# Kernel optimization log

Hardware: AMD Instinct MI355X
Metric: run time of the kernel (lower is better)

The kernel has to match this reference:

```python
import jax, jax.numpy as jnp
import numpy as np

DIM = 768
NUM_HEADS = 12
HEAD_DIM = DIM // NUM_HEADS
SCALE = HEAD_DIM ** -0.5
B, N = 8, 1024


def setup_inputs() -> dict:
    key = jax.random.key(0)
    k1, k2, k3, k4, k5 = jax.random.split(key, 5)
    x = jax.random.normal(k1, (B, N, DIM), dtype=jnp.float32)
    # qkv: Linear(dim, 3*dim, bias=False); proj: Linear(dim, dim) with bias
    w_qkv = jax.random.normal(k2, (3 * DIM, DIM), dtype=jnp.float32) * (DIM ** -0.5)
    w_proj = jax.random.normal(k3, (DIM, DIM), dtype=jnp.float32) * (DIM ** -0.5)
    b_proj = jnp.zeros((DIM,), dtype=jnp.float32)
    # learned attention mask parameter, shape (H, L, L) with L >= N
    att_mask = jax.random.normal(k4, (NUM_HEADS, N, N), dtype=jnp.float32)
    return {"x": x, "w_qkv": w_qkv, "w_proj": w_proj, "b_proj": b_proj, "att_mask": att_mask}


def reference(x, w_qkv, w_proj, b_proj, att_mask):
    Bx, Nx, C = x.shape
    # qkv projection -> (3, B, H, N, head_dim)
    qkv = (x @ w_qkv.T).reshape(Bx, Nx, 3, NUM_HEADS, C // NUM_HEADS)
    qkv = jnp.transpose(qkv, (2, 0, 3, 1, 4))
    q, k, v = qkv[0], qkv[1], qkv[2]  # gpd_ratio==active_ratio==1 -> scaling factor 1
    # scores [B, H, N, N]
    attn = jnp.einsum('bhnd,bhmd->bhnm', q, k) * SCALE
    # custom sigmoid mask gating before softmax (broadcast over batch)
    attn = attn * jax.nn.sigmoid(att_mask[:, :Nx, :Nx])[None, :, :, :]
    attn = jax.nn.softmax(attn, axis=-1)
    out = jnp.einsum('bhnm,bhmd->bhnd', attn, v)
    out = jnp.transpose(out, (0, 2, 1, 3)).reshape(Bx, Nx, C)
    return out @ w_proj.T + b_proj
```

## Files before the change

### kernel.cpp

```cpp
#include <hip/hip_runtime.h>
#include <math.h>
#include <stdint.h>

typedef unsigned short u16;
typedef __attribute__((ext_vector_type(8))) short short8;
typedef __attribute__((ext_vector_type(4))) float f32x4;

#define GATE_SCALE 0.18033688011112042f

#if __has_builtin(__builtin_amdgcn_exp2f)
#define FEXP2(x) __builtin_amdgcn_exp2f(x)
#else
#define FEXP2(x) exp2f(x)
#endif

__device__ __forceinline__ u16 f2b(float f) {
    union { float f; unsigned u; } v; v.f = f;
    unsigned r = v.u + 0x7fffu + ((v.u >> 16) & 1u);
    return (u16)(r >> 16);
}
__device__ __forceinline__ u16 f2b_hu(float f) {
    union { float f; unsigned u; } v; v.f = f;
    return (u16)((v.u + 0x8000u) >> 16);
}
__device__ __forceinline__ float b2f(u16 u) {
    union { float f; unsigned u; } v; v.u = ((unsigned)u) << 16; return v.f;
}

#define GLL16(gsrc, ldsbase) __builtin_amdgcn_global_load_lds(                    \
    (__attribute__((address_space(1))) void*)(uintptr_t)(gsrc),                   \
    (__attribute__((address_space(3))) void*)(uint32_t)(uintptr_t)(ldsbase),      \
    16, 0, 0)

#define NX4  1572864
#define NW14 442368
#define NW24 147456
#define NXW4 (NX4 + NW14 + NW24)

__global__ __launch_bounds__(256) void prep_all(
    const float4* __restrict__ x, const float4* __restrict__ wq,
    const float4* __restrict__ wp,
    ushort4* __restrict__ xb, ushort4* __restrict__ wqb,
    ushort4* __restrict__ wpb,
    const float4* __restrict__ mask4, u16* __restrict__ gp)
{
    __shared__ u16 L[64][72];
    const int bx = blockIdx.x;
    const int t = threadIdx.x;

    if (bx >= 3072) {
        size_t i = (size_t)(bx - 3072) * 256 + t;
        float4 v; ushort4* dst; size_t j;
        if (i < NX4)            { j = i;               v = x[j];  dst = xb;  }
        else if (i < NX4 + NW14){ j = i - NX4;         v = wq[j]; dst = wqb; }
        else                    { j = i - (NX4 + NW14);v = wp[j]; dst = wpb; }
        ushort4 o; o.x = f2b(v.x); o.y = f2b(v.y); o.z = f2b(v.z); o.w = f2b(v.w);
        dst[j] = o;
        return;
    }

    const int bid = bx;
    const int kt = bid & 15, qt = (bid >> 4) & 15, h = bid >> 8;

    #pragma unroll
    for (int s = 0; s < 4; ++s) {
        const int idx = t + s * 256;
        const int row = idx >> 4, c4 = idx & 15;
        float4 v = mask4[(size_t)(h * 1024 + qt * 64 + row) * 256 + kt * 16 + c4];
        L[row][c4 * 4 + 0] = f2b(GATE_SCALE / (1.f + __expf(-v.x)));
        L[row][c4 * 4 + 1] = f2b(GATE_SCALE / (1.f + __expf(-v.y)));
        L[row][c4 * 4 + 2] = f2b(GATE_SCALE / (1.f + __expf(-v.z)));
        L[row][c4 * 4 + 3] = f2b(GATE_SCALE / (1.f + __expf(-v.w)));
    }
    __syncthreads();

    const int w = t >> 6, l = t & 63;
    const int fq = l >> 4, fr = l & 15;
    union { u16 u[16]; float4 f[2]; } vals;
    #pragma unroll
    for (int i = 0; i < 4; ++i)
        #pragma unroll
        for (int nt = 0; nt < 4; ++nt)
            vals.u[i * 4 + nt] = L[16 * w + 4 * fq + i][nt * 16 + fr];
    float4* dst = (float4*)(gp + (size_t)bid * 4096 + (size_t)t * 16);
    dst[0] = vals.f[0];
    dst[1] = vals.f[1];
}

__global__ __launch_bounds__(256) void qkv_gemm(
    const u16* __restrict__ xb, const u16* __restrict__ wb,
    u16* __restrict__ qb, u16* __restrict__ kb, u16* __restrict__ vb)
{
    __shared__ u16 As[2][4096];
    __shared__ u16 Bs[2][4096];
    const int t = threadIdx.x, l = t & 63, w = t >> 6;
    const int wm = (w & 1) * 64, wn = (w >> 1) * 64;

    const int orig = blockIdx.x + 18 * blockIdx.y;
    const int nid = (orig & 7) * 144 + (orig >> 3);
    const int m0 = (nid / 18) * 128, c0 = (nid % 18) * 128;

    f32x4 acc[4][4];
    #pragma unroll
    for (int i = 0; i < 4; ++i)
        #pragma unroll
        for (int j = 0; j < 4; ++j) { f32x4 z = {0.f,0.f,0.f,0.f}; acc[i][j] = z; }

    const int srow = l >> 2, sseg = l & 3;
    const int gcol = ((sseg ^ ((srow >> 1) & 3)) << 3);
    const u16* a0 = xb + (size_t)(m0 + w * 16 + srow) * 768 + gcol;
    const u16* a1 = a0 + (size_t)64 * 768;
    const u16* b0p = wb + (size_t)(c0 + w * 16 + srow) * 768 + gcol;
    const u16* b1p = b0p + (size_t)64 * 768;
    const int wofs = w * 512;

    const int fr = l & 15, fq = l >> 4;
    const int fseg = (fq ^ ((fr >> 1) & 3)) << 3;

    auto stage = [&](int bi, int koff) {
        GLL16(a0 + koff, &As[bi][wofs]);
        GLL16(a1 + koff, &As[bi][2048 + wofs]);
        GLL16(b0p + koff, &Bs[bi][wofs]);
        GLL16(b1p + koff, &Bs[bi][2048 + wofs]);
    };

    stage(0, 0);

    for (int kt = 0; kt < 24; ++kt) {
        asm volatile("s_waitcnt vmcnt(0)" ::: "memory");
        __builtin_amdgcn_s_barrier();
        if (kt < 23) stage((kt + 1) & 1, (kt + 1) * 32);
        const u16* A = As[kt & 1];
        const u16* B = Bs[kt & 1];
        short8 af[4], bf[4];
        #pragma unroll
        for (int mt = 0; mt < 4; ++mt)
            af[mt] = *(const short8*)&A[(wm + mt * 16 + fr) * 32 + fseg];
        #pragma unroll
        for (int nt = 0; nt < 4; ++nt)
            bf[nt] = *(const short8*)&B[(wn + nt * 16 + fr) * 32 + fseg];
        #pragma unroll
        for (int mt = 0; mt < 4; ++mt)
            #pragma unroll
            for (int nt = 0; nt < 4; ++nt)
                acc[mt][nt] = __builtin_amdgcn_mfma_f32_16x16x32_bf16(
                    af[mt], bf[nt], acc[mt][nt], 0, 0, 0);
    }

    const int b = m0 >> 10;
    const int n0 = m0 & 1023;
    #pragma unroll
    for (int nt = 0; nt < 4; ++nt) {
        const int c = c0 + wn + nt * 16 + fr;
        const int which = c / 768;
        const int rem = c - which * 768;
        const int h = rem >> 6, d = rem & 63;
        if (which < 2) {
            u16* dst = ((which == 0) ? qb : kb)
                       + ((size_t)(b * 12 + h) * 1024) * 64 + d;
            #pragma unroll
            for (int mt = 0; mt < 4; ++mt)
                #pragma unroll
                for (int r = 0; r < 4; ++r) {
                    const int n = n0 + wm + mt * 16 + fq * 4 + r;
                    dst[(size_t)n * 64] = f2b(acc[mt][nt][r]);
                }
        } else {
            u16* dst = vb + ((size_t)(b * 12 + h) * 64 + d) * 1024
                          + n0 + wm + fq * 4;
            #pragma unroll
            for (int mt = 0; mt < 4; ++mt) {
                ushort4 pk;
                pk.x = f2b(acc[mt][nt][0]); pk.y = f2b(acc[mt][nt][1]);
                pk.z = f2b(acc[mt][nt][2]); pk.w = f2b(acc[mt][nt][3]);
                *(ushort4*)(dst + mt * 16) = pk;
            }
        }
    }
}

__global__ __launch_bounds__(256, 3) void flash_attn(
    const u16* __restrict__ qb, const u16* __restrict__ kb,
    const u16* __restrict__ vt, const u16* __restrict__ gperm,
    u16* __restrict__ aob)
{
    __shared__ u16 Ks[2][4096], Vts[2][4096], Ps[4096];
    const int t = threadIdx.x, l = t & 63, w = t >> 6;
    const int bid = blockIdx.x;
    const int xcd = bid & 7, jj = bid >> 3;
    const int bh = (jj % 12) * 8 + xcd;
    const int qtb = jj / 12;
    const int h = bh % 12, b = bh / 12;
    const int q0 = qtb * 128;

    const u16* hq = qb + (size_t)bh * 65536;
    const u16* hk = kb + (size_t)bh * 65536;
    const u16* hv = vt + (size_t)bh * 65536;
    const u16* hgb = gperm + ((size_t)h * 256 + qtb * 32) * 4096 + (w * 64 + l) * 16;

    const int sr = l >> 3, ss = l & 7;
    const int sg = ((ss ^ (sr & 7)) << 3);
    const int j0 = w * 2, j1 = j0 + 1;

    const int fq = l >> 4, fr = l & 15;
    const int sega = ((fq ^ (fr & 7)) << 3);
    const int segb = (((4 + fq) ^ (fr & 7)) << 3);

    short8 aq[2][2];
    #pragma unroll
    for (int qh = 0; qh < 2; ++qh) {
        const u16* qrow = hq + (size_t)(q0 + qh * 64 + 16 * w + fr) * 64;
        aq[qh][0] = *(const short8*)(qrow + fq * 8);
        aq[qh][1] = *(const short8*)(qrow + 32 + fq * 8);
    }

    GLL16(hk + (size_t)(j0 * 8 + sr) * 64 + sg, &Ks[0][j0 * 512]);
    GLL16(hk + (size_t)(j1 * 8 + sr) * 64 + sg, &Ks[0][j1 * 512]);
    GLL16(hv + (size_t)(j0 * 8 + sr) * 1024 + sg, &Vts[0][j0 * 512]);
    GLL16(hv + (size_t)(j1 * 8 + sr) * 1024 + sg, &Vts[0][j1 * 512]);
    __builtin_amdgcn_sched_barrier(0);

    short8 gn[4];
    gn[0] = *(const short8*)(hgb);
    gn[1] = *(const short8*)(hgb + 8);
    gn[2] = *(const short8*)(hgb + 65536);
    gn[3] = *(const short8*)(hgb + 65536 + 8);

    float l_part[2][4] = {{0.f,0.f,0.f,0.f},{0.f,0.f,0.f,0.f}};
    f32x4 o[2][4];
    #pragma unroll
    for (int qh = 0; qh < 2; ++qh)
        #pragma unroll
        for (int nt = 0; nt < 4; ++nt) { f32x4 z = {0.f,0.f,0.f,0.f}; o[qh][nt] = z; }

    for (int kt = 0; kt < 16; ++kt) {
        asm volatile("s_waitcnt vmcnt(4)" ::: "memory");
        __builtin_amdgcn_s_barrier();

        if (kt < 15) {
            const size_t ko = (size_t)(kt + 1) * 64;
            u16* kd = &Ks[(kt + 1) & 1][0];
            u16* vd = &Vts[(kt + 1) & 1][0];
            GLL16(hk + (ko + j0 * 8 + sr) * 64 + sg, kd + j0 * 512);
            GLL16(hk + (ko + j1 * 8 + sr) * 64 + sg, kd + j1 * 512);
            GLL16(hv + (size_t)(j0 * 8 + sr) * 1024 + ko + sg, vd + j0 * 512);
            GLL16(hv + (size_t)(j1 * 8 + sr) * 1024 + ko + sg, vd + j1 * 512);
            __builtin_amdgcn_sched_barrier(0);
        }

        short8 g[4];
        #pragma unroll
        for (int s = 0; s < 4; ++s) g[s] = gn[s];
        if (kt < 15) {
            const size_t go = (size_t)(kt + 1) * 4096;
            gn[0] = *(const short8*)(hgb + go);
            gn[1] = *(const short8*)(hgb + go + 8);
            gn[2] = *(const short8*)(hgb + 65536 + go);
            gn[3] = *(const short8*)(hgb + 65536 + go + 8);
        }

        const u16* KS = &Ks[kt & 1][0];
        const u16* VS = &Vts[kt & 1][0];

        f32x4 sv[2][4];
        __builtin_amdgcn_s_setprio(1);
        #pragma unroll
        for (int nt = 0; nt < 4; ++nt) {
            short8 kf0 = *(const short8*)&KS[(nt * 16 + fr) * 64 + sega];
            short8 kf1 = *(const short8*)&KS[(nt * 16 + fr) * 64 + segb];
            f32x4 z0 = {0.f,0.f,0.f,0.f};
            z0 = __builtin_amdgcn_mfma_f32_16x16x32_bf16(aq[0][0], kf0, z0, 0, 0, 0);
            z0 = __builtin_amdgcn_mfma_f32_16x16x32_bf16(aq[0][1], kf1, z0, 0, 0, 0);
            sv[0][nt] = z0;
            f32x4 z1 = {0.f,0.f,0.f,0.f};
            z1 = __builtin_amdgcn_mfma_f32_16x16x32_bf16(aq[1][0], kf0, z1, 0, 0, 0);
            z1 = __builtin_amdgcn_mfma_f32_16x16x32_bf16(aq[1][1], kf1, z1, 0, 0, 0);
            sv[1][nt] = z1;
        }
        __builtin_amdgcn_s_setprio(0);

        short8 ap[2][2];
        #pragma unroll
        for (int qh = 0; qh < 2; ++qh) {
            #pragma unroll
            for (int i = 0; i < 4; ++i) {
                const int pr = 4 * fq + i;
                #pragma unroll
                for (int nt = 0; nt < 4; ++nt) {
                    const int idx = i * 4 + nt;
                    const float gv = b2f((u16)(idx < 8 ? g[2 * qh][idx]
                                                       : g[2 * qh + 1][idx - 8]));
                    const float p = FEXP2(sv[qh][nt][i] * gv);
                    l_part[qh][i] += p;
                    const int col = nt * 16 + fr;
                    Ps[w * 1024 + pr * 64 + (((col >> 3) ^ (pr & 7)) << 3) + (col & 7)]
                        = f2b_hu(p);
                }
            }
            ap[qh][0] = *(const short8*)&Ps[w * 1024 + fr * 64 + sega];
            ap[qh][1] = *(const short8*)&Ps[w * 1024 + fr * 64 + segb];
        }

        __builtin_amdgcn_s_setprio(1);
        #pragma unroll
        for (int nt = 0; nt < 4; ++nt) {
            short8 vf0 = *(const short8*)&VS[(nt * 16 + fr) * 64 + sega];
            short8 vf1 = *(const short8*)&VS[(nt * 16 + fr) * 64 + segb];
            o[0][nt] = __builtin_amdgcn_mfma_f32_16x16x32_bf16(ap[0][0], vf0, o[0][nt], 0, 0, 0);
            o[0][nt] = __builtin_amdgcn_mfma_f32_16x16x32_bf16(ap[0][1], vf1, o[0][nt], 0, 0, 0);
            o[1][nt] = __builtin_amdgcn_mfma_f32_16x16x32_bf16(ap[1][0], vf0, o[1][nt], 0, 0, 0);
            o[1][nt] = __builtin_amdgcn_mfma_f32_16x16x32_bf16(ap[1][1], vf1, o[1][nt], 0, 0, 0);
        }
        __builtin_amdgcn_s_setprio(0);
    }

    #pragma unroll
    for (int qh = 0; qh < 2; ++qh) {
        #pragma unroll
        for (int i = 0; i < 4; ++i) {
            float s = l_part[qh][i];
            s += __shfl_xor(s, 1, 16);
            s += __shfl_xor(s, 2, 16);
            s += __shfl_xor(s, 4, 16);
            s += __shfl_xor(s, 8, 16);
            const float inv = 1.f / s;
            const int n = q0 + qh * 64 + 16 * w + 4 * fq + i;
            const size_t rowoff = ((size_t)b * 1024 + n) * 768 + h * 64;
            #pragma unroll
            for (int nt = 0; nt < 4; ++nt)
                aob[rowoff + nt * 16 + fr] = f2b(o[qh][nt][i] * inv);
        }
    }
}

__global__ __launch_bounds__(256, 2) void proj_gemm(
    const u16* __restrict__ aob, const u16* __restrict__ wb,
    const float* __restrict__ bproj, float* __restrict__ out)
{
    __shared__ u16 As[3][4096];
    __shared__ u16 Bs[3][8192];
    const int t = threadIdx.x, l = t & 63, w = t >> 6;
    const int wc = w * 64;

    const int orig = blockIdx.x;
    const int nid = (orig & 7) * 24 + (orig >> 3);
    const int m0 = (nid / 3) * 128, c0 = (nid % 3) * 256;

    f32x4 acc[8][4];
    #pragma unroll
    for (int i = 0; i < 8; ++i)
        #pragma unroll
        for (int j = 0; j < 4; ++j) { f32x4 z = {0.f,0.f,0.f,0.f}; acc[i][j] = z; }

    const int srow = l >> 2, sseg = l & 3;
    const int gcol = ((sseg ^ ((srow >> 1) & 3)) << 3);
    const u16* aA = aob + (size_t)(m0 + w * 16 + srow) * 768 + gcol;
    const u16* aB = wb + (size_t)(c0 + w * 16 + srow) * 768 + gcol;

    const int fr = l & 15, fq = l >> 4;
    const int fseg = (fq ^ ((fr >> 1) & 3)) << 3;

    auto stage = [&](int bi, int koff) {
        GLL16(aA + koff,                      &As[bi][(w + 0) * 512]);
        GLL16(aA + koff + (size_t)64 * 768,   &As[bi][(w + 4) * 512]);
        GLL16(aB + koff,                      &Bs[bi][(w + 0) * 512]);
        GLL16(aB + koff + (size_t)64 * 768,   &Bs[bi][(w + 4) * 512]);
        GLL16(aB + koff + (size_t)128 * 768,  &Bs[bi][(w + 8) * 512]);
        GLL16(aB + koff + (size_t)192 * 768,  &Bs[bi][(w + 12) * 512]);
    };

    stage(0, 0);
    stage(1, 32);

    int cur = 0;
    for (int kt = 0; kt < 24; ++kt) {
        if (kt < 23) asm volatile("s_waitcnt vmcnt(6)" ::: "memory");
        else         asm volatile("s_waitcnt vmcnt(0)" ::: "memory");
        __builtin_amdgcn_s_barrier();
        if (kt < 22) {
            const int nn = (cur == 0) ? 2 : cur - 1;
            stage(nn, (kt + 2) * 32);
        }
        const u16* A = As[cur];
        const u16* B = Bs[cur];
        short8 af[8], bf[4];
        #pragma unroll
        for (int mt = 0; mt < 8; ++mt)
            af[mt] = *(const short8*)&A[(mt * 16 + fr) * 32 + fseg];
        #pragma unroll
        for (int nt = 0; nt < 4; ++nt)
            bf[nt] = *(const short8*)&B[(wc + nt * 16 + fr) * 32 + fseg];
        #pragma unroll
        for (int mt = 0; mt < 8; ++mt)
            #pragma unroll
            for (int nt = 0; nt < 4; ++nt)
                acc[mt][nt] = __builtin_amdgcn_mfma_f32_16x16x32_bf16(
                    af[mt], bf[nt], acc[mt][nt], 0, 0, 0);
        cur = (cur == 2) ? 0 : cur + 1;
    }

    #pragma unroll
    for (int nt = 0; nt < 4; ++nt) {
        const int c = c0 + wc + nt * 16 + fr;
        const float bias = bproj[c];
        #pragma unroll
        for (int mt = 0; mt < 8; ++mt)
            #pragma unroll
            for (int r = 0; r < 4; ++r) {
                const int m = m0 + mt * 16 + fq * 4 + r;
                out[(size_t)m * 768 + c] = acc[mt][nt][r] + bias;
            }
    }
}

extern "C" void kernel_launch(void* const* d_in, const int* in_sizes, int n_in,
                              void* d_out, int out_size, void* d_ws, size_t ws_size,
                              hipStream_t stream)
{
    const float* x     = (const float*)d_in[0];
    const float* wqkv  = (const float*)d_in[1];
    const float* wproj = (const float*)d_in[2];
    const float* bproj = (const float*)d_in[3];
    const float* mask  = (const float*)d_in[4];
    float* out = (float*)d_out;

    char* ws = (char*)d_ws;
    u16* gperm  = (u16*)(ws);
    u16* xb     = (u16*)(ws + 25165824);
    u16* wqkvb  = (u16*)(ws + 37748736);
    u16* wprojb = (u16*)(ws + 41287680);
    u16* qb     = (u16*)(ws + 42467328);
    u16* kb     = (u16*)(ws + 55050240);
    u16* vb     = (u16*)(ws + 67633152);
    u16* aob    = (u16*)(ws + 80216064);

    prep_all<<<3072 + NXW4 / 256, 256, 0, stream>>>(
        (const float4*)x, (const float4*)wqkv, (const float4*)wproj,
        (ushort4*)xb, (ushort4*)wqkvb, (ushort4*)wprojb,
        (const float4*)mask, gperm);

    qkv_gemm<<<dim3(18, 64), 256, 0, stream>>>(xb, wqkvb, qb, kb, vb);

    flash_attn<<<768, 256, 0, stream>>>(qb, kb, vb, gperm, aob);

    proj_gemm<<<192, 256, 0, stream>>>(aob, wprojb, bproj, out);
}
```

Baseline: 230.7 us.

## Fuse sigmoid mask gating into attention kernel, drop gate precompute pass

Removes the mask-prep stage that precomputed a permuted bf16 sigmoid gate. The attention kernel now loads the fp32 mask directly and computes the scaled sigmoid inline with exp2 and a fast reciprocal. This saves a separate kernel's read and write traffic, but each batch re-reads the fp32 mask with strided scalar loads and recomputes the sigmoid. It also raises register pressure, with 64 float registers held for the gate prefetch.

```diff
diff --git a/kernel.cpp b/kernel.cpp
--- a/kernel.cpp
+++ b/kernel.cpp
@@ -7,6 +7,7 @@
 typedef __attribute__((ext_vector_type(4))) float f32x4;
 
 #define GATE_SCALE 0.18033688011112042f
+#define LOG2E 1.4426950408889634f
 
 #if __has_builtin(__builtin_amdgcn_exp2f)
 #define FEXP2(x) __builtin_amdgcn_exp2f(x)
@@ -14,6 +15,15 @@
 #define FEXP2(x) exp2f(x)
 #endif
 
+__device__ __forceinline__ float fsig(float m) {
+    float e = FEXP2(m * -LOG2E);
+#if __has_builtin(__builtin_amdgcn_rcpf)
+    return GATE_SCALE * __builtin_amdgcn_rcpf(1.f + e);
+#else
+    return GATE_SCALE / (1.f + e);
+#endif
+}
+
 __device__ __forceinline__ u16 f2b(float f) {
     union { float f; unsigned u; } v; v.f = f;
     unsigned r = v.u + 0x7fffu + ((v.u >> 16) & 1u);
@@ -23,9 +33,6 @@
     union { float f; unsigned u; } v; v.f = f;
     return (u16)((v.u + 0x8000u) >> 16);
 }
-__device__ __forceinline__ float b2f(u16 u) {
-    union { float f; unsigned u; } v; v.u = ((unsigned)u) << 16; return v.f;
-}
 
 #define GLL16(gsrc, ldsbase) __builtin_amdgcn_global_load_lds(                    \
     (__attribute__((address_space(1))) void*)(uintptr_t)(gsrc),                   \
@@ -37,54 +44,19 @@
 #define NW24 147456
 #define NXW4 (NX4 + NW14 + NW24)
 
-__global__ __launch_bounds__(256) void prep_all(
+__global__ __launch_bounds__(256) void prep_xw(
     const float4* __restrict__ x, const float4* __restrict__ wq,
     const float4* __restrict__ wp,
     ushort4* __restrict__ xb, ushort4* __restrict__ wqb,
-    ushort4* __restrict__ wpb,
-    const float4* __restrict__ mask4, u16* __restrict__ gp)
+    ushort4* __restrict__ wpb)
 {
-    __shared__ u16 L[64][72];
-    const int bx = blockIdx.x;
-    const int t = threadIdx.x;
-
-    if (bx >= 3072) {
-        size_t i = (size_t)(bx - 3072) * 256 + t;
-        float4 v; ushort4* dst; size_t j;
-        if (i < NX4)            { j = i;               v = x[j];  dst = xb;  }
-        else if (i < NX4 + NW14){ j = i - NX4;         v = wq[j]; dst = wqb; }
-        else                    { j = i - (NX4 + NW14);v = wp[j]; dst = wpb; }
-        ushort4 o; o.x = f2b(v.x); o.y = f2b(v.y); o.z = f2b(v.z); o.w = f2b(v.w);
-        dst[j] = o;
-        return;
-    }
-
-    const int bid = bx;
-    const int kt = bid & 15, qt = (bid >> 4) & 15, h = bid >> 8;
-
-    #pragma unroll
-    for (int s = 0; s < 4; ++s) {
-        const int idx = t + s * 256;
-        const int row = idx >> 4, c4 = idx & 15;
-        float4 v = mask4[(size_t)(h * 1024 + qt * 64 + row) * 256 + kt * 16 + c4];
-        L[row][c4 * 4 + 0] = f2b(GATE_SCALE / (1.f + __expf(-v.x)));
-        L[row][c4 * 4 + 1] = f2b(GATE_SCALE / (1.f + __expf(-v.y)));
-        L[row][c4 * 4 + 2] = f2b(GATE_SCALE / (1.f + __expf(-v.z)));
-        L[row][c4 * 4 + 3] = f2b(GATE_SCALE / (1.f + __expf(-v.w)));
-    }
-    __syncthreads();
-
-    const int w = t >> 6, l = t & 63;
-    const int fq = l >> 4, fr = l & 15;
-    union { u16 u[16]; float4 f[2]; } vals;
-    #pragma unroll
-    for (int i = 0; i < 4; ++i)
-        #pragma unroll
-        for (int nt = 0; nt < 4; ++nt)
-            vals.u[i * 4 + nt] = L[16 * w + 4 * fq + i][nt * 16 + fr];
-    float4* dst = (float4*)(gp + (size_t)bid * 4096 + (size_t)t * 16);
-    dst[0] = vals.f[0];
-    dst[1] = vals.f[1];
+    size_t i = (size_t)blockIdx.x * 256 + threadIdx.x;
+    float4 v; ushort4* dst; size_t j;
+    if (i < NX4)            { j = i;               v = x[j];  dst = xb;  }
+    else if (i < NX4 + NW14){ j = i - NX4;         v = wq[j]; dst = wqb; }
+    else                    { j = i - (NX4 + NW14);v = wp[j]; dst = wpb; }
+    ushort4 o; o.x = f2b(v.x); o.y = f2b(v.y); o.z = f2b(v.z); o.w = f2b(v.w);
+    dst[j] = o;
 }
 
 __global__ __launch_bounds__(256) void qkv_gemm(
@@ -181,7 +153,7 @@
 
 __global__ __launch_bounds__(256, 3) void flash_attn(
     const u16* __restrict__ qb, const u16* __restrict__ kb,
-    const u16* __restrict__ vt, const u16* __restrict__ gperm,
+    const u16* __restrict__ vt, const float* __restrict__ mask,
     u16* __restrict__ aob)
 {
     __shared__ u16 Ks[2][4096], Vts[2][4096], Ps[4096];
@@ -196,7 +168,6 @@
     const u16* hq = qb + (size_t)bh * 65536;
     const u16* hk = kb + (size_t)bh * 65536;
     const u16* hv = vt + (size_t)bh * 65536;
-    const u16* hgb = gperm + ((size_t)h * 256 + qtb * 32) * 4096 + (w * 64 + l) * 16;
 
     const int sr = l >> 3, ss = l & 7;
     const int sg = ((ss ^ (sr & 7)) << 3);
@@ -205,6 +176,18 @@
     const int fq = l >> 4, fr = l & 15;
     const int sega = ((fq ^ (fr & 7)) << 3);
     const int segb = (((4 + fq) ^ (fr & 7)) << 3);
+
+    const float* hm = mask + ((size_t)h * 1024 + q0 + 16 * w) * 1024 + fr;
+    auto gload = [&](float* dst, int ktv) {
+        #pragma unroll
+        for (int qh = 0; qh < 2; ++qh)
+            #pragma unroll
+            for (int i = 0; i < 4; ++i)
+                #pragma unroll
+                for (int nt = 0; nt < 4; ++nt)
+                    dst[qh * 16 + i * 4 + nt] =
+                        hm[(size_t)(qh * 64 + 4 * fq + i) * 1024 + ktv * 64 + nt * 16];
+    };
 
     short8 aq[2][2];
     #pragma unroll
@@ -220,11 +203,8 @@
     GLL16(hv + (size_t)(j1 * 8 + sr) * 1024 + sg, &Vts[0][j1 * 512]);
     __builtin_amdgcn_sched_barrier(0);
 
-    short8 gn[4];
-    gn[0] = *(const short8*)(hgb);
-    gn[1] = *(const short8*)(hgb + 8);
-    gn[2] = *(const short8*)(hgb + 65536);
-    gn[3] = *(const short8*)(hgb + 65536 + 8);
+    float gn[32];
+    gload(gn, 0);
 
     float l_part[2][4] = {{0.f,0.f,0.f,0.f},{0.f,0.f,0.f,0.f}};
     f32x4 o[2][4];
@@ -234,7 +214,7 @@
         for (int nt = 0; nt < 4; ++nt) { f32x4 z = {0.f,0.f,0.f,0.f}; o[qh][nt] = z; }
 
     for (int kt = 0; kt < 16; ++kt) {
-        asm volatile("s_waitcnt vmcnt(4)" ::: "memory");
+        asm volatile("s_waitcnt vmcnt(32)" ::: "memory");
         __builtin_amdgcn_s_barrier();
 
         if (kt < 15) {
@@ -248,16 +228,10 @@
             __builtin_amdgcn_sched_barrier(0);
         }
 
-        short8 g[4];
-        #pragma unroll
-        for (int s = 0; s < 4; ++s) g[s] = gn[s];
-        if (kt < 15) {
-            const size_t go = (size_t)(kt + 1) * 4096;
-            gn[0] = *(const short8*)(hgb + go);
-            gn[1] = *(const short8*)(hgb + go + 8);
-            gn[2] = *(const short8*)(hgb + 65536 + go);
-            gn[3] = *(const short8*)(hgb + 65536 + go + 8);
-        }
+        float g[32];
+        #pragma unroll
+        for (int s = 0; s < 32; ++s) g[s] = gn[s];
+        if (kt < 15) gload(gn, kt + 1);
 
         const u16* KS = &Ks[kt & 1][0];
         const u16* VS = &Vts[kt & 1][0];
@@ -287,9 +261,7 @@
                 const int pr = 4 * fq + i;
                 #pragma unroll
                 for (int nt = 0; nt < 4; ++nt) {
-                    const int idx = i * 4 + nt;
-                    const float gv = b2f((u16)(idx < 8 ? g[2 * qh][idx]
-                                                       : g[2 * qh + 1][idx - 8]));
+                    const float gv = fsig(g[qh * 16 + i * 4 + nt]);
                     const float p = FEXP2(sv[qh][nt][i] * gv);
                     l_part[qh][i] += p;
                     const int col = nt * 16 + fr;
@@ -425,7 +397,6 @@
     float* out = (float*)d_out;
 
     char* ws = (char*)d_ws;
-    u16* gperm  = (u16*)(ws);
     u16* xb     = (u16*)(ws + 25165824);
     u16* wqkvb  = (u16*)(ws + 37748736);
     u16* wprojb = (u16*)(ws + 41287680);
@@ -434,14 +405,13 @@
     u16* vb     = (u16*)(ws + 67633152);
     u16* aob    = (u16*)(ws + 80216064);
 
-    prep_all<<<3072 + NXW4 / 256, 256, 0, stream>>>(
+    prep_xw<<<NXW4 / 256, 256, 0, stream>>>(
         (const float4*)x, (const float4*)wqkv, (const float4*)wproj,
-        (ushort4*)xb, (ushort4*)wqkvb, (ushort4*)wprojb,
-        (const float4*)mask, gperm);
+        (ushort4*)xb, (ushort4*)wqkvb, (ushort4*)wprojb);
 
     qkv_gemm<<<dim3(18, 64), 256, 0, stream>>>(xb, wqkvb, qb, kb, vb);
 
-    flash_attn<<<768, 256, 0, stream>>>(qb, kb, vb, gperm, aob);
+    flash_attn<<<768, 256, 0, stream>>>(qb, kb, vb, mask, aob);
 
     proj_gemm<<<192, 256, 0, stream>>>(aob, wprojb, bproj, out);
 }
```

New measurement: 272.7 us. 1.18x slower.
